# Kernel tuning notes

Hardware: AMD Instinct MI355X
Metric: run time of the kernel (lower is better)

## Reference

```python
import jax, jax.numpy as jnp
import numpy as np

B, TQ, TK, D, H = 2, 2048, 2048, 1024, 16


def setup_inputs() -> dict:
    key = jax.random.key(0)
    ks = jax.random.split(key, 8)
    s = 1.0 / np.sqrt(D)
    x_q = jax.random.normal(ks[0], (B, TQ, D), jnp.float32)
    x_k = jax.random.normal(ks[1], (B, TK, D), jnp.float32)
    x_v = jax.random.normal(ks[2], (B, TK, D), jnp.float32)
    # causal mask, True = masked (matches masked_fill semantics)
    causal = jnp.triu(jnp.ones((TQ, TK), jnp.bool_), k=1)
    attn_mask = jnp.broadcast_to(causal, (B, TQ, TK))
    Wq = jax.random.normal(ks[3], (D, D), jnp.float32) * s
    Wk = jax.random.normal(ks[4], (D, D), jnp.float32) * s
    Wv = jax.random.normal(ks[5], (D, D), jnp.float32) * s
    Wo = jax.random.normal(ks[6], (D, D), jnp.float32) * s
    z = jnp.zeros((D,), jnp.float32)
    return {"x_q": x_q, "x_k": x_k, "x_v": x_v, "attn_mask": attn_mask,
            "Wq": Wq, "bq": z, "Wk": Wk, "bk": z, "Wv": Wv, "bv": z,
            "Wo": Wo, "bo": z, "n_heads": H}


def reference(x_q, x_k, x_v, attn_mask, Wq, bq, Wk, bk, Wv, bv, Wo, bo, n_heads):
    Bv, Tq, Dm = x_q.shape
    Tk = x_k.shape[1]
    dh = Dm // n_heads
    # nn.Linear: y = x @ W^T + b; split heads -> [B, H, T, dh]
    Q = (jnp.einsum('btd,od->bto', x_q, Wq) + bq).reshape(Bv, Tq, n_heads, dh).transpose(0, 2, 1, 3)
    K = (jnp.einsum('btd,od->bto', x_k, Wk) + bk).reshape(Bv, Tk, n_heads, dh).transpose(0, 2, 1, 3)
    V = (jnp.einsum('btd,od->bto', x_v, Wv) + bv).reshape(Bv, Tk, n_heads, dh).transpose(0, 2, 1, 3)
    scale = 1.0 / np.sqrt(dh).astype(np.float32)
    scores = jnp.einsum('bhqd,bhkd->bhqk', Q, K) * scale  # [B,H,Tq,Tk]
    scores = jnp.where(attn_mask[:, None, :, :], -jnp.inf, scores)
    A = jax.nn.softmax(scores, axis=-1)  # dropout p=0.0 -> identity
    out = jnp.einsum('bhqk,bhkd->bhqd', A, V)
    out = out.transpose(0, 2, 1, 3).reshape(Bv, Tq, Dm)
    return jnp.einsum('btd,od->bto', out, Wo) + bo
```

## Files before the change

### kernel.cpp

```cpp
#include <hip/hip_runtime.h>


typedef __attribute__((ext_vector_type(8))) __bf16 bf16x8;
typedef __attribute__((ext_vector_type(4))) float f32x4;
typedef unsigned short u16;

constexpr int BATCH  = 2;
constexpr int TSEQ   = 2048;
constexpr int DMODEL = 1024;
constexpr int NHEAD  = 16;
constexpr int DHEAD  = 64;
constexpr int MROWS  = BATCH * TSEQ;

static __device__ __forceinline__ u16 f2bf(float f) {
  union { float f; unsigned int u; } v; v.f = f;
  unsigned int u = v.u;
  return (u16)((u + 0x7fffu + ((u >> 16) & 1u)) >> 16);
}

static __device__ __forceinline__ void gload16(const void* g, void* l) {
  __builtin_amdgcn_global_load_lds(
      (const __attribute__((address_space(1))) void*)g,
      (__attribute__((address_space(3))) void*)l, 16, 0, 0);
}

__global__ __launch_bounds__(256) void cvt_multi(const float* __restrict__ s0,
                                                 const float* __restrict__ s1,
                                                 const float* __restrict__ s2,
                                                 const float* __restrict__ s3,
                                                 u16* __restrict__ d0, u16* __restrict__ d1,
                                                 u16* __restrict__ d2, u16* __restrict__ d3,
                                                 int n4) {
  const float* s; u16* d;
  switch (blockIdx.y) {
    case 0: s = s0; d = d0; break;
    case 1: s = s1; d = d1; break;
    case 2: s = s2; d = d2; break;
    default: s = s3; d = d3; break;
  }
  int i = blockIdx.x * 256 + threadIdx.x;
  if (i >= n4) return;
  float4 f = ((const float4*)s)[i];
  ushort4 o;
  o.x = f2bf(f.x); o.y = f2bf(f.y); o.z = f2bf(f.z); o.w = f2bf(f.w);
  ((ushort4*)d)[i] = o;
}

template <typename Epi>
static __device__ __forceinline__ void gemm_body(const u16* __restrict__ X_,
                                                 const u16* __restrict__ W_,
                                                 const float* __restrict__ bias,
                                                 Epi epi) {
  __shared__ __align__(16) u16 As[2][4096];
  __shared__ __align__(16) u16 Bs[2][4096];
  const int lane = threadIdx.x & 63, wave = threadIdx.x >> 6;
  const int l16 = lane & 15, lk = lane >> 4;
  const int wm = wave >> 2, wn = wave & 3;
  const int row0 = blockIdx.x * 128, col0 = blockIdx.y * 128;
  constexpr int K = DMODEL;
  const u16* ga = X_ + (size_t)(row0 + wave * 16 + l16) * K + lk * 8;
  const u16* gb = W_ + (size_t)(col0 + wave * 16 + l16) * K + lk * 8;
  f32x4 acc[4][2];
#pragma unroll
  for (int mt = 0; mt < 4; ++mt)
#pragma unroll
    for (int nt = 0; nt < 2; ++nt) acc[mt][nt] = (f32x4){0.f, 0.f, 0.f, 0.f};
  gload16(ga, &As[0][wave * 512]);
  gload16(gb, &Bs[0][wave * 512]);
  __syncthreads();
  int buf = 0;
  for (int ks = 0; ks < K / 32; ++ks) {
    if (ks + 1 < K / 32) {
      gload16(ga + (ks + 1) * 32, &As[buf ^ 1][wave * 512]);
      gload16(gb + (ks + 1) * 32, &Bs[buf ^ 1][wave * 512]);
    }
    bf16x8 a[4], b[2];
#pragma unroll
    for (int mt = 0; mt < 4; ++mt)
      a[mt] = *(const bf16x8*)&As[buf][(wm * 4 + mt) * 512 + lane * 8];
#pragma unroll
    for (int nt = 0; nt < 2; ++nt)
      b[nt] = *(const bf16x8*)&Bs[buf][(wn * 2 + nt) * 512 + lane * 8];
#pragma unroll
    for (int mt = 0; mt < 4; ++mt)
#pragma unroll
      for (int nt = 0; nt < 2; ++nt)
        acc[mt][nt] =
            __builtin_amdgcn_mfma_f32_16x16x32_bf16(a[mt], b[nt], acc[mt][nt], 0, 0, 0);
    __syncthreads();
    buf ^= 1;
  }
#pragma unroll
  for (int mt = 0; mt < 4; ++mt)
#pragma unroll
    for (int nt = 0; nt < 2; ++nt)
#pragma unroll
      for (int r = 0; r < 4; ++r) {
        int m = row0 + wm * 64 + mt * 16 + lk * 4 + r;
        int n = col0 + wn * 32 + nt * 16 + l16;
        float v = acc[mt][nt][r] + bias[n];
        epi(m, n, v);
      }
}

__global__ __launch_bounds__(512) void gemm_qkv(
    const u16* __restrict__ xq, const u16* __restrict__ xk, const u16* __restrict__ xv,
    const u16* __restrict__ wq, const u16* __restrict__ wk, const u16* __restrict__ wv,
    const float* __restrict__ bq, const float* __restrict__ bk, const float* __restrict__ bv,
    u16* __restrict__ Qh, u16* __restrict__ Kh, u16* __restrict__ Vt) {
  const int z = blockIdx.z;
  const u16* X = z == 0 ? xq : (z == 1 ? xk : xv);
  const u16* W = z == 0 ? wq : (z == 1 ? wk : wv);
  const float* bias = z == 0 ? bq : (z == 1 ? bk : bv);
  u16* O01 = z == 0 ? Qh : Kh;
  gemm_body(X, W, bias, [&](int m, int n, float v) {
    int bb = m >> 11, t = m & (TSEQ - 1);
    int h = n >> 6, dd = n & (DHEAD - 1);
    if (z == 0) v *= 0.125f;
    if (z == 2)
      Vt[(((size_t)(bb * NHEAD + h)) * DHEAD + dd) * TSEQ + t] = f2bf(v);
    else
      O01[(((size_t)(bb * NHEAD + h)) * TSEQ + t) * DHEAD + dd] = f2bf(v);
  });
}

__global__ __launch_bounds__(512) void gemm_o(const u16* __restrict__ AO,
                                              const u16* __restrict__ wo,
                                              const float* __restrict__ bias,
                                              float* __restrict__ out) {
  gemm_body(AO, wo, bias,
            [&](int m, int n, float v) { out[(size_t)m * DMODEL + n] = v; });
}

__global__ __launch_bounds__(512, 6) void flash_attn(const u16* __restrict__ Qh,
                                                     const u16* __restrict__ Kh,
                                                     const u16* __restrict__ Vt,
                                                     u16* __restrict__ AO) {
  const int lane = threadIdx.x & 63, wave = threadIdx.x >> 6;
  const int l16 = lane & 15, lk = lane >> 4;
  const int bh = blockIdx.x;
  const int qt = (gridDim.y - 1) - blockIdx.y;
  const int q0 = qt * 128;
  const int b = bh >> 4, h = bh & 15;

  __shared__ __align__(16) u16 Kl[2][4096];
  __shared__ __align__(16) u16 Vl[2][4096];
  __shared__ __align__(16) u16 plds[8][16][72];

  const u16* Qb = Qh + (size_t)bh * TSEQ * DHEAD;
  const u16* Kb = Kh + (size_t)bh * TSEQ * DHEAD;
  const u16* Vb = Vt + (size_t)bh * DHEAD * TSEQ;

  bf16x8 qf[2];
  {
    const u16* qp = Qb + (size_t)(q0 + wave * 16 + l16) * DHEAD + lk * 8;
    qf[0] = *(const bf16x8*)(qp);
    qf[1] = *(const bf16x8*)(qp + 32);
  }

  float mrow[4], lsum[4];
  f32x4 acco[4];
#pragma unroll
  for (int r = 0; r < 4; ++r) { mrow[r] = -1e30f; lsum[r] = 0.f; }
#pragma unroll
  for (int dt = 0; dt < 4; ++dt) acco[dt] = (f32x4){0.f, 0.f, 0.f, 0.f};

  auto stage_kv = [&](int bufi, int kbase) {
    int trow = (wave >> 1) * 16 + l16;
    int dhs = (wave & 1) * 4 + lk;
    gload16(Kb + (size_t)(kbase + trow) * DHEAD + dhs * 8, &Kl[bufi][wave * 512]);
    gload16(Vb + (size_t)trow * TSEQ + kbase + dhs * 8, &Vl[bufi][wave * 512]);
  };

  const int nkb = 2 * qt + 2;
  const int kbdiag = 2 * qt + (wave >> 2);
  stage_kv(0, 0);
  __syncthreads();
  int buf = 0;
  const int qrow_base = q0 + wave * 16 + 4 * lk;

  for (int kb = 0; kb < nkb; ++kb) {
    const int kbase = kb * 64;
    if (kb + 1 < nkb) stage_kv(buf ^ 1, kbase + 64);

    if (kb <= kbdiag) {
      f32x4 s[4];
#pragma unroll
      for (int nt = 0; nt < 4; ++nt) {
        bf16x8 k0f = *(const bf16x8*)&Kl[buf][nt * 1024 + lane * 8];
        bf16x8 k1f = *(const bf16x8*)&Kl[buf][nt * 1024 + 512 + lane * 8];
        f32x4 z = (f32x4){0.f, 0.f, 0.f, 0.f};
        z = __builtin_amdgcn_mfma_f32_16x16x32_bf16(qf[0], k0f, z, 0, 0, 0);
        z = __builtin_amdgcn_mfma_f32_16x16x32_bf16(qf[1], k1f, z, 0, 0, 0);
        s[nt] = z;
      }
      if (kb == kbdiag) {
#pragma unroll
        for (int nt = 0; nt < 4; ++nt)
#pragma unroll
          for (int r = 0; r < 4; ++r) {
            int kcol = kbase + nt * 16 + l16;
            s[nt][r] = (kcol <= qrow_base + r) ? s[nt][r] : -1e30f;
          }
      }
      float pmax[4];
      bool need = false;
#pragma unroll
      for (int r = 0; r < 4; ++r) {
        pmax[r] = fmaxf(fmaxf(s[0][r], s[1][r]), fmaxf(s[2][r], s[3][r]));
        need |= (pmax[r] > mrow[r] + 8.f);
      }
      if (__any(need)) {
#pragma unroll
        for (int r = 0; r < 4; ++r) {
          float mx = pmax[r];
#pragma unroll
          for (int off = 1; off < 16; off <<= 1) mx = fmaxf(mx, __shfl_xor(mx, off, 16));
          float mnew = fmaxf(mrow[r], mx);
          float alpha = __expf(mrow[r] - mnew);
          lsum[r] *= alpha;
#pragma unroll
          for (int dt = 0; dt < 4; ++dt) acco[dt][r] *= alpha;
          mrow[r] = mnew;
        }
      }
#pragma unroll
      for (int r = 0; r < 4; ++r)
#pragma unroll
        for (int nt = 0; nt < 4; ++nt) {
          float p = __expf(s[nt][r] - mrow[r]);
          s[nt][r] = p;
          lsum[r] += p;
        }
#pragma unroll
      for (int nt = 0; nt < 4; ++nt)
#pragma unroll
        for (int r = 0; r < 4; ++r)
          plds[wave][4 * lk + r][nt * 16 + l16] = f2bf(s[nt][r]);
      bf16x8 pf0 = *(const bf16x8*)&plds[wave][l16][lk * 8];
      bf16x8 pf1 = *(const bf16x8*)&plds[wave][l16][32 + lk * 8];
#pragma unroll
      for (int dt = 0; dt < 4; ++dt) {
        bf16x8 v0 = *(const bf16x8*)&Vl[buf][dt * 1024 + lane * 8];
        bf16x8 v1 = *(const bf16x8*)&Vl[buf][dt * 1024 + 512 + lane * 8];
        acco[dt] = __builtin_amdgcn_mfma_f32_16x16x32_bf16(pf0, v0, acco[dt], 0, 0, 0);
        acco[dt] = __builtin_amdgcn_mfma_f32_16x16x32_bf16(pf1, v1, acco[dt], 0, 0, 0);
      }
    }
    __syncthreads();
    buf ^= 1;
  }

#pragma unroll
  for (int r = 0; r < 4; ++r) {
    float t = lsum[r];
#pragma unroll
    for (int off = 1; off < 16; off <<= 1) t += __shfl_xor(t, off, 16);
    lsum[r] = 1.f / t;
  }
#pragma unroll
  for (int dt = 0; dt < 4; ++dt)
#pragma unroll
    for (int r = 0; r < 4; ++r) {
      int t = qrow_base + r;
      int col = h * DHEAD + dt * 16 + l16;
      AO[((size_t)(b * TSEQ + t)) * DMODEL + col] = f2bf(acco[dt][r] * lsum[r]);
    }
}

extern "C" void kernel_launch(void* const* d_in, const int* in_sizes, int n_in,
                              void* d_out, int out_size, void* d_ws, size_t ws_size,
                              hipStream_t stream) {
  const float* x_q = (const float*)d_in[0];
  const float* x_k = (const float*)d_in[1];
  const float* x_v = (const float*)d_in[2];
  const float* Wq = (const float*)d_in[4];
  const float* bq = (const float*)d_in[5];
  const float* Wk = (const float*)d_in[6];
  const float* bk = (const float*)d_in[7];
  const float* Wv = (const float*)d_in[8];
  const float* bv = (const float*)d_in[9];
  const float* Wo = (const float*)d_in[10];
  const float* bo = (const float*)d_in[11];

  const size_t nx = (size_t)MROWS * DMODEL;
  const size_t nw = (size_t)DMODEL * DMODEL;
  u16* ws   = (u16*)d_ws;
  u16* xq_b = ws;
  u16* xk_b = xq_b + nx;
  u16* xv_b = xk_b + nx;
  u16* wq_b = xv_b + nx;
  u16* wk_b = wq_b + nw;
  u16* wv_b = wk_b + nw;
  u16* wo_b = wv_b + nw;
  u16* Qh   = wo_b + nw;
  u16* Kh   = Qh + nx;
  u16* Vt   = Kh + nx;
  u16* AO   = Vt + nx;

  const int n4x = (int)(nx / 4), n4w = (int)(nw / 4);
  cvt_multi<<<dim3((n4x + 255) / 256, 3), 256, 0, stream>>>(
      x_q, x_k, x_v, nullptr, xq_b, xk_b, xv_b, nullptr, n4x);
  cvt_multi<<<dim3((n4w + 255) / 256, 4), 256, 0, stream>>>(
      Wq, Wk, Wv, Wo, wq_b, wk_b, wv_b, wo_b, n4w);

  gemm_qkv<<<dim3(MROWS / 128, DMODEL / 128, 3), 512, 0, stream>>>(
      xq_b, xk_b, xv_b, wq_b, wk_b, wv_b, bq, bk, bv, Qh, Kh, Vt);

  flash_attn<<<dim3(BATCH * NHEAD, TSEQ / 128), 512, 0, stream>>>(Qh, Kh, Vt, AO);

  gemm_o<<<dim3(MROWS / 128, DMODEL / 128), 512, 0, stream>>>(AO, wo_b, bo, (float*)d_out);
}
```

Before: 158.2 us.

## Shrink attention and output-projection tiles, drop LDS staging, use exp2 softmax

The attention kernel moves from 128-query, 8-wave blocks to 64-query, 4-wave blocks. It drops the shared-memory K/V double buffer and its barriers and loads K and V fragments straight from global memory into registers. Softmax switches to exp2 by folding log2(e) into the Q scale, and the rescale threshold is loosened. The output projection gets a new 256-thread, 128x64-tile GEMM variant. Together these aim for more blocks and higher occupancy, at the cost of more uncoalesced global loads and less K/V reuse across waves.

```diff
diff --git a/kernel.cpp b/kernel.cpp
--- a/kernel.cpp
+++ b/kernel.cpp
@@ -47,10 +47,10 @@
 }
 
 template <typename Epi>
-static __device__ __forceinline__ void gemm_body(const u16* __restrict__ X_,
-                                                 const u16* __restrict__ W_,
-                                                 const float* __restrict__ bias,
-                                                 Epi epi) {
+static __device__ __forceinline__ void gemm_body8(const u16* __restrict__ X_,
+                                                  const u16* __restrict__ W_,
+                                                  const float* __restrict__ bias,
+                                                  Epi epi) {
   __shared__ __align__(16) u16 As[2][4096];
   __shared__ __align__(16) u16 Bs[2][4096];
   const int lane = threadIdx.x & 63, wave = threadIdx.x >> 6;
@@ -103,6 +103,67 @@
       }
 }
 
+template <typename Epi>
+static __device__ __forceinline__ void gemm_body4(const u16* __restrict__ X_,
+                                                  const u16* __restrict__ W_,
+                                                  const float* __restrict__ bias,
+                                                  Epi epi) {
+  constexpr int K = DMODEL;
+  __shared__ __align__(16) u16 As[2][8 * 512];
+  __shared__ __align__(16) u16 Bs[2][4 * 512];
+  const int lane = threadIdx.x & 63, wave = threadIdx.x >> 6;
+  const int l16 = lane & 15, lk = lane >> 4;
+  const int wm = wave >> 1, wn = wave & 1;
+  const int row0 = blockIdx.x * 128, col0 = blockIdx.y * 64;
+  const u16* ga = X_ + (size_t)(row0 + l16) * K + lk * 8;
+  const u16* gb = W_ + (size_t)(col0 + l16) * K + lk * 8;
+  f32x4 acc[4][2];
+#pragma unroll
+  for (int mt = 0; mt < 4; ++mt)
+#pragma unroll
+    for (int nt = 0; nt < 2; ++nt) acc[mt][nt] = (f32x4){0.f, 0.f, 0.f, 0.f};
+  auto stage = [&](int bufi, int ks) {
+#pragma unroll
+    for (int j = 0; j < 2; ++j) {
+      int s = j * 4 + wave;
+      gload16(ga + (size_t)s * 16 * K + ks * 32, &As[bufi][s * 512]);
+    }
+    gload16(gb + (size_t)wave * 16 * K + ks * 32, &Bs[bufi][wave * 512]);
+  };
+  stage(0, 0);
+  __syncthreads();
+  int buf = 0;
+  for (int ks = 0; ks < K / 32; ++ks) {
+    if (ks + 1 < K / 32) stage(buf ^ 1, ks + 1);
+    bf16x8 a[4], b[2];
+#pragma unroll
+    for (int mt = 0; mt < 4; ++mt)
+      a[mt] = *(const bf16x8*)&As[buf][(wm * 4 + mt) * 512 + lane * 8];
+#pragma unroll
+    for (int nt = 0; nt < 2; ++nt)
+      b[nt] = *(const bf16x8*)&Bs[buf][(wn * 2 + nt) * 512 + lane * 8];
+#pragma unroll
+    for (int mt = 0; mt < 4; ++mt)
+#pragma unroll
+      for (int nt = 0; nt < 2; ++nt)
+        acc[mt][nt] =
+            __builtin_amdgcn_mfma_f32_16x16x32_bf16(a[mt], b[nt], acc[mt][nt], 0, 0, 0);
+    __syncthreads();
+    buf ^= 1;
+  }
+#pragma unroll
+  for (int mt = 0; mt < 4; ++mt)
+#pragma unroll
+    for (int nt = 0; nt < 2; ++nt)
+#pragma unroll
+      for (int r = 0; r < 4; ++r) {
+        int m = row0 + wm * 64 + mt * 16 + lk * 4 + r;
+        int n = col0 + wn * 32 + nt * 16 + l16;
+        float v = acc[mt][nt][r] + bias[n];
+        epi(m, n, v);
+      }
+}
+
 __global__ __launch_bounds__(512) void gemm_qkv(
     const u16* __restrict__ xq, const u16* __restrict__ xk, const u16* __restrict__ xv,
     const u16* __restrict__ wq, const u16* __restrict__ wk, const u16* __restrict__ wv,
@@ -113,10 +174,10 @@
   const u16* W = z == 0 ? wq : (z == 1 ? wk : wv);
   const float* bias = z == 0 ? bq : (z == 1 ? bk : bv);
   u16* O01 = z == 0 ? Qh : Kh;
-  gemm_body(X, W, bias, [&](int m, int n, float v) {
+  gemm_body8(X, W, bias, [&](int m, int n, float v) {
     int bb = m >> 11, t = m & (TSEQ - 1);
     int h = n >> 6, dd = n & (DHEAD - 1);
-    if (z == 0) v *= 0.125f;
+    if (z == 0) v *= 0.18033688011112042f;
     if (z == 2)
       Vt[(((size_t)(bb * NHEAD + h)) * DHEAD + dd) * TSEQ + t] = f2bf(v);
     else
@@ -124,15 +185,15 @@
   });
 }
 
-__global__ __launch_bounds__(512) void gemm_o(const u16* __restrict__ AO,
-                                              const u16* __restrict__ wo,
-                                              const float* __restrict__ bias,
-                                              float* __restrict__ out) {
-  gemm_body(AO, wo, bias,
-            [&](int m, int n, float v) { out[(size_t)m * DMODEL + n] = v; });
-}
-
-__global__ __launch_bounds__(512, 6) void flash_attn(const u16* __restrict__ Qh,
+__global__ __launch_bounds__(256, 4) void gemm_o(const u16* __restrict__ AO,
+                                                 const u16* __restrict__ wo,
+                                                 const float* __restrict__ bias,
+                                                 float* __restrict__ out) {
+  gemm_body4(AO, wo, bias,
+             [&](int m, int n, float v) { out[(size_t)m * DMODEL + n] = v; });
+}
+
+__global__ __launch_bounds__(256, 4) void flash_attn(const u16* __restrict__ Qh,
                                                      const u16* __restrict__ Kh,
                                                      const u16* __restrict__ Vt,
                                                      u16* __restrict__ AO) {
@@ -140,12 +201,10 @@
   const int l16 = lane & 15, lk = lane >> 4;
   const int bh = blockIdx.x;
   const int qt = (gridDim.y - 1) - blockIdx.y;
-  const int q0 = qt * 128;
+  const int q0 = qt * 64;
   const int b = bh >> 4, h = bh & 15;
 
-  __shared__ __align__(16) u16 Kl[2][4096];
-  __shared__ __align__(16) u16 Vl[2][4096];
-  __shared__ __align__(16) u16 plds[8][16][72];
+  __shared__ __align__(16) u16 plds[4][16][72];
 
   const u16* Qb = Qh + (size_t)bh * TSEQ * DHEAD;
   const u16* Kb = Kh + (size_t)bh * TSEQ * DHEAD;
@@ -165,90 +224,79 @@
 #pragma unroll
   for (int dt = 0; dt < 4; ++dt) acco[dt] = (f32x4){0.f, 0.f, 0.f, 0.f};
 
-  auto stage_kv = [&](int bufi, int kbase) {
-    int trow = (wave >> 1) * 16 + l16;
-    int dhs = (wave & 1) * 4 + lk;
-    gload16(Kb + (size_t)(kbase + trow) * DHEAD + dhs * 8, &Kl[bufi][wave * 512]);
-    gload16(Vb + (size_t)trow * TSEQ + kbase + dhs * 8, &Vl[bufi][wave * 512]);
-  };
-
-  const int nkb = 2 * qt + 2;
-  const int kbdiag = 2 * qt + (wave >> 2);
-  stage_kv(0, 0);
-  __syncthreads();
-  int buf = 0;
   const int qrow_base = q0 + wave * 16 + 4 * lk;
+  const int nkb = qt + 1;
 
   for (int kb = 0; kb < nkb; ++kb) {
     const int kbase = kb * 64;
-    if (kb + 1 < nkb) stage_kv(buf ^ 1, kbase + 64);
-
-    if (kb <= kbdiag) {
-      f32x4 s[4];
+    f32x4 s[4];
+#pragma unroll
+    for (int nt = 0; nt < 4; ++nt) {
+      const u16* kp = Kb + (size_t)(kbase + nt * 16 + l16) * DHEAD + lk * 8;
+      bf16x8 k0f = *(const bf16x8*)(kp);
+      bf16x8 k1f = *(const bf16x8*)(kp + 32);
+      f32x4 z = (f32x4){0.f, 0.f, 0.f, 0.f};
+      z = __builtin_amdgcn_mfma_f32_16x16x32_bf16(qf[0], k0f, z, 0, 0, 0);
+      z = __builtin_amdgcn_mfma_f32_16x16x32_bf16(qf[1], k1f, z, 0, 0, 0);
+      s[nt] = z;
+    }
+    bf16x8 v0f[4], v1f[4];
+#pragma unroll
+    for (int dt = 0; dt < 4; ++dt) {
+      const u16* vp = Vb + (size_t)(dt * 16 + l16) * TSEQ + kbase + lk * 8;
+      v0f[dt] = *(const bf16x8*)(vp);
+      v1f[dt] = *(const bf16x8*)(vp + 32);
+    }
+    if (kb == qt) {
+#pragma unroll
+      for (int nt = 0; nt < 4; ++nt)
+#pragma unroll
+        for (int r = 0; r < 4; ++r) {
+          int kcol = kbase + nt * 16 + l16;
+          s[nt][r] = (kcol <= qrow_base + r) ? s[nt][r] : -1e30f;
+        }
+    }
+    float pmax[4];
+    bool need = false;
+#pragma unroll
+    for (int r = 0; r < 4; ++r) {
+      pmax[r] = fmaxf(fmaxf(s[0][r], s[1][r]), fmaxf(s[2][r], s[3][r]));
+      need |= (pmax[r] > mrow[r] + 12.f);
+    }
+    if (__any(need)) {
+#pragma unroll
+      for (int r = 0; r < 4; ++r) {
+        float mx = pmax[r];
+#pragma unroll
+        for (int off = 1; off < 16; off <<= 1) mx = fmaxf(mx, __shfl_xor(mx, off, 16));
+        float mnew = fmaxf(mrow[r], mx);
+        float alpha = exp2f(mrow[r] - mnew);
+        lsum[r] *= alpha;
+#pragma unroll
+        for (int dt = 0; dt < 4; ++dt) acco[dt][r] *= alpha;
+        mrow[r] = mnew;
+      }
+    }
+#pragma unroll
+    for (int r = 0; r < 4; ++r)
 #pragma unroll
       for (int nt = 0; nt < 4; ++nt) {
-        bf16x8 k0f = *(const bf16x8*)&Kl[buf][nt * 1024 + lane * 8];
-        bf16x8 k1f = *(const bf16x8*)&Kl[buf][nt * 1024 + 512 + lane * 8];
-        f32x4 z = (f32x4){0.f, 0.f, 0.f, 0.f};
-        z = __builtin_amdgcn_mfma_f32_16x16x32_bf16(qf[0], k0f, z, 0, 0, 0);
-        z = __builtin_amdgcn_mfma_f32_16x16x32_bf16(qf[1], k1f, z, 0, 0, 0);
-        s[nt] = z;
+        float p = exp2f(s[nt][r] - mrow[r]);
+        s[nt][r] = p;
+        lsum[r] += p;
       }
-      if (kb == kbdiag) {
-#pragma unroll
-        for (int nt = 0; nt < 4; ++nt)
-#pragma unroll
-          for (int r = 0; r < 4; ++r) {
-            int kcol = kbase + nt * 16 + l16;
-            s[nt][r] = (kcol <= qrow_base + r) ? s[nt][r] : -1e30f;
-          }
-      }
-      float pmax[4];
-      bool need = false;
-#pragma unroll
-      for (int r = 0; r < 4; ++r) {
-        pmax[r] = fmaxf(fmaxf(s[0][r], s[1][r]), fmaxf(s[2][r], s[3][r]));
-        need |= (pmax[r] > mrow[r] + 8.f);
-      }
-      if (__any(need)) {
-#pragma unroll
-        for (int r = 0; r < 4; ++r) {
-          float mx = pmax[r];
-#pragma unroll
-          for (int off = 1; off < 16; off <<= 1) mx = fmaxf(mx, __shfl_xor(mx, off, 16));
-          float mnew = fmaxf(mrow[r], mx);
-          float alpha = __expf(mrow[r] - mnew);
-          lsum[r] *= alpha;
-#pragma unroll
-          for (int dt = 0; dt < 4; ++dt) acco[dt][r] *= alpha;
-          mrow[r] = mnew;
-        }
-      }
+#pragma unroll
+    for (int nt = 0; nt < 4; ++nt)
 #pragma unroll
       for (int r = 0; r < 4; ++r)
-#pragma unroll
-        for (int nt = 0; nt < 4; ++nt) {
-          float p = __expf(s[nt][r] - mrow[r]);
-          s[nt][r] = p;
-          lsum[r] += p;
-        }
-#pragma unroll
-      for (int nt = 0; nt < 4; ++nt)
-#pragma unroll
-        for (int r = 0; r < 4; ++r)
-          plds[wave][4 * lk + r][nt * 16 + l16] = f2bf(s[nt][r]);
-      bf16x8 pf0 = *(const bf16x8*)&plds[wave][l16][lk * 8];
-      bf16x8 pf1 = *(const bf16x8*)&plds[wave][l16][32 + lk * 8];
-#pragma unroll
-      for (int dt = 0; dt < 4; ++dt) {
-        bf16x8 v0 = *(const bf16x8*)&Vl[buf][dt * 1024 + lane * 8];
-        bf16x8 v1 = *(const bf16x8*)&Vl[buf][dt * 1024 + 512 + lane * 8];
-        acco[dt] = __builtin_amdgcn_mfma_f32_16x16x32_bf16(pf0, v0, acco[dt], 0, 0, 0);
-        acco[dt] = __builtin_amdgcn_mfma_f32_16x16x32_bf16(pf1, v1, acco[dt], 0, 0, 0);
-      }
-    }
-    __syncthreads();
-    buf ^= 1;
+        plds[wave][4 * lk + r][nt * 16 + l16] = f2bf(s[nt][r]);
+    bf16x8 pf0 = *(const bf16x8*)&plds[wave][l16][lk * 8];
+    bf16x8 pf1 = *(const bf16x8*)&plds[wave][l16][32 + lk * 8];
+#pragma unroll
+    for (int dt = 0; dt < 4; ++dt) {
+      acco[dt] = __builtin_amdgcn_mfma_f32_16x16x32_bf16(pf0, v0f[dt], acco[dt], 0, 0, 0);
+      acco[dt] = __builtin_amdgcn_mfma_f32_16x16x32_bf16(pf1, v1f[dt], acco[dt], 0, 0, 0);
+    }
   }
 
 #pragma unroll
@@ -307,7 +355,7 @@
   gemm_qkv<<<dim3(MROWS / 128, DMODEL / 128, 3), 512, 0, stream>>>(
       xq_b, xk_b, xv_b, wq_b, wk_b, wv_b, bq, bk, bv, Qh, Kh, Vt);
 
-  flash_attn<<<dim3(BATCH * NHEAD, TSEQ / 128), 512, 0, stream>>>(Qh, Kh, Vt, AO);
-
-  gemm_o<<<dim3(MROWS / 128, DMODEL / 128), 512, 0, stream>>>(AO, wo_b, bo, (float*)d_out);
-}
+  flash_attn<<<dim3(BATCH * NHEAD, TSEQ / 64), 256, 0, stream>>>(Qh, Kh, Vt, AO);
+
+  gemm_o<<<dim3(MROWS / 128, DMODEL / 64), 256, 0, stream>>>(AO, wo_b, bo, (float*)d_out);
+}
```

New measurement: 251.0 us. 58.7% more time.
